# Kernel optimization log

Measured on AMD Instinct MI355X. Metric: run time of the kernel, lower is better.

The kernel has to match this reference:

```python
import jax, jax.numpy as jnp
import numpy as np

B, S, H = 32, 2048, 1024
STDV = 0.1


def setup_inputs() -> dict:
    key = jax.random.key(0)
    ks = jax.random.split(key, 8)
    u = lambda k, shape: jax.random.uniform(k, shape, minval=-STDV, maxval=STDV, dtype=jnp.float32)
    return {
        "inputs": jax.random.normal(ks[0], (B, S, H), dtype=jnp.float32),
        "qvector": jax.random.normal(ks[1], (B, H), dtype=jnp.float32),
        "W_u_1": u(ks[2], (H, H)),
        "W_u_m_1": u(ks[3], (H, H)),
        "W_u_h_1": u(ks[4], (H, 1)),
        "W_u_2": u(ks[5], (H, H)),
        "W_u_m_2": u(ks[6], (H, H)),
        "W_u_h_2": u(ks[7], (H, 1)),
    }


def reference(inputs, qvector, W_u_1, W_u_m_1, W_u_h_1, W_u_2, W_u_m_2, W_u_h_2):
    # inputs: [B, S, H], qvector: [B, H]
    def hop(m, W, Wm, Wh):
        # M = tanh(inputs @ W) gated by tanh(m @ Wm)  -> [B, S, H]
        M = jnp.tanh(jnp.einsum("bsh,hd->bsd", inputs, W))
        M = M * jnp.tanh(m @ Wm)[:, None, :]
        U = jnp.einsum("bsd,do->bso", M, Wh)        # [B, S, 1]
        alpha = jax.nn.softmax(U, axis=1)           # softmax over sequence
        return jnp.sum(inputs * alpha, axis=1)      # [B, H]

    mean_in = jnp.mean(inputs, axis=1)              # [B, H]
    u_att0 = mean_in
    m0 = mean_in * qvector
    u_att1 = hop(m0, W_u_1, W_u_m_1, W_u_h_1)
    m1 = m0 + u_att0 * qvector
    u_att2 = hop(m1, W_u_2, W_u_m_2, W_u_h_2)
    # original returns list [u_att0, u_att1, u_att2]; stack for a single array
    return jnp.stack([u_att0, u_att1, u_att2])      # [3, B, H]
```

## Files before the change

kernel.cpp:

```cpp
#include <hip/hip_runtime.h>
#include <hip/hip_bf16.h>
#include <math.h>

#define B_  32
#define S_  2048
#define H_  1024
#define M_TOT (B_ * S_)

typedef __bf16 bf16x8 __attribute__((ext_vector_type(8)));
typedef float  f32x4  __attribute__((ext_vector_type(4)));

__device__ __forceinline__ unsigned short f2bf(float f) {
    union { float f; unsigned int u; } v; v.f = f;
    unsigned int u = v.u;
    return (unsigned short)((u + 0x7fffu + ((u >> 16) & 1u)) >> 16);
}

__device__ __forceinline__ float bf2f(unsigned short s) {
    return __uint_as_float(((unsigned int)s) << 16);
}

__device__ __forceinline__ float fast_tanh(float x) {
    float e = __expf(2.0f * x);
    return 1.0f - 2.0f / (e + 1.0f);
}

__global__ void k_meanconv(const float* __restrict__ x,
                           unsigned short* __restrict__ xbf,
                           float* __restrict__ meanOut ) {
    int b  = blockIdx.x;
    int sc = blockIdx.y;
    int t  = threadIdx.x;
    size_t base = ((size_t)b * S_ + (size_t)sc * 32) * H_;
    const float4* xr = (const float4*)(x + base);
    ushort4* xo = (ushort4*)(xbf + base);
    float a0 = 0.f, a1 = 0.f, a2 = 0.f, a3 = 0.f;
    for (int s = 0; s < 32; ++s) {
        float4 v = xr[(size_t)s * 256 + t];
        a0 += v.x; a1 += v.y; a2 += v.z; a3 += v.w;
        ushort4 o;
        o.x = f2bf(v.x); o.y = f2bf(v.y); o.z = f2bf(v.z); o.w = f2bf(v.w);
        xo[(size_t)s * 256 + t] = o;
    }
    const float scl = 1.0f / (float)S_;
    float* mp = meanOut + b * H_ + t * 4;
    atomicAdd(mp + 0, a0 * scl);
    atomicAdd(mp + 1, a1 * scl);
    atomicAdd(mp + 2, a2 * scl);
    atomicAdd(mp + 3, a3 * scl);
}

__global__ void k_wconv(const float* __restrict__ W1,
                        const float* __restrict__ W2,
                        unsigned short* __restrict__ WT) {
    int n = blockIdx.x;
    int t = threadIdx.x;
    const float* src = (n < H_) ? (W1 + n) : (W2 + (n - H_));
    unsigned short* dst = WT + (size_t)n * H_;
    for (int kk = 0; kk < 4; ++kk) {
        int k = t + kk * 256;
        dst[k] = f2bf(src[(size_t)k * H_]);
    }
}

__global__ void k_vpart(const float* __restrict__ meanIn,
                        const float* __restrict__ q,
                        const float* __restrict__ Wm1,
                        const float* __restrict__ Wm2,
                        float* __restrict__ vtmp ) {
    int b   = blockIdx.x;
    int hop = blockIdx.y;
    int hc  = blockIdx.z;
    int t   = threadIdx.x;
    __shared__ float mL[128];
    float scale = (hop == 0) ? 1.0f : 2.0f;
    int h0 = hc * 128;
    if (t < 128)
        mL[t] = meanIn[b * H_ + h0 + t] * q[b * H_ + h0 + t] * scale;
    __syncthreads();
    const float* Wm = hop ? Wm2 : Wm1;
    int d0 = t * 4;
    float a0 = 0.f, a1 = 0.f, a2 = 0.f, a3 = 0.f;
    for (int h = 0; h < 128; ++h) {
        float m = mL[h];
        float4 w = *(const float4*)(Wm + (size_t)(h0 + h) * H_ + d0);
        a0 += m * w.x; a1 += m * w.y; a2 += m * w.z; a3 += m * w.w;
    }
    float* vo = vtmp + b * 2048 + hop * H_ + d0;
    atomicAdd(vo + 0, a0);
    atomicAdd(vo + 1, a1);
    atomicAdd(vo + 2, a2);
    atomicAdd(vo + 3, a3);
}

__global__ void k_vfin(const float* __restrict__ vtmp,
                       const float* __restrict__ Wh1,
                       const float* __restrict__ Wh2,
                       float* __restrict__ vcat) {
    int i = blockIdx.x * 256 + threadIdx.x;
    int hop = (i >> 10) & 1;
    int d = i & 1023;
    const float* Wh = hop ? Wh2 : Wh1;
    vcat[i] = tanhf(vtmp[i]) * Wh[d];
}

__global__ __launch_bounds__(256) void k_gemm(const unsigned short* __restrict__ Xbf,
                                              const unsigned short* __restrict__ WT,
                                              const float* __restrict__ vcat,
                                              float* __restrict__ U ) {
    int nt = blockIdx.x;
    int mt = blockIdx.y;
    int m0 = mt * 128;
    int n0 = nt * 128;
    int t    = threadIdx.x;
    int lane = t & 63;
    int wave = t >> 6;
    int wm = wave >> 1, wn = wave & 1;
    int fr = lane & 15;
    int fq = lane >> 4;

    __shared__ unsigned short As[128 * 32];
    __shared__ unsigned short Bs[128 * 32];

    f32x4 acc[4][4];
#pragma unroll
    for (int i = 0; i < 4; ++i)
#pragma unroll
        for (int j = 0; j < 4; ++j)
#pragma unroll
            for (int r = 0; r < 4; ++r) acc[i][j][r] = 0.0f;

    int idx0 = t, idx1 = t + 256;
    int row0 = idx0 >> 2, kc0 = ((idx0 & 3) - ((row0 >> 1) & 3)) & 3;
    int row1 = idx1 >> 2, kc1 = ((idx1 & 3) - ((row1 >> 1) & 3)) & 3;
    const unsigned short* gA0 = Xbf + (size_t)(m0 + row0) * H_ + kc0 * 8;
    const unsigned short* gA1 = Xbf + (size_t)(m0 + row1) * H_ + kc1 * 8;
    const unsigned short* gB0 = WT  + (size_t)(n0 + row0) * H_ + kc0 * 8;
    const unsigned short* gB1 = WT  + (size_t)(n0 + row1) * H_ + kc1 * 8;
    unsigned short* lA0 = As + idx0 * 8;
    unsigned short* lA1 = As + idx1 * 8;
    unsigned short* lB0 = Bs + idx0 * 8;
    unsigned short* lB1 = Bs + idx1 * 8;

    int slotR = (fq + ((fr >> 1) & 3)) & 3;
    const bf16x8* pa[4];
    const bf16x8* pb[4];
#pragma unroll
    for (int i = 0; i < 4; ++i)
        pa[i] = (const bf16x8*)(As + ((wm * 64 + i * 16 + fr) * 4 + slotR) * 8);
#pragma unroll
    for (int j = 0; j < 4; ++j)
        pb[j] = (const bf16x8*)(Bs + ((wn * 64 + j * 16 + fr) * 4 + slotR) * 8);

    for (int k0 = 0; k0 < H_; k0 += 32) {
        __builtin_amdgcn_global_load_lds((const __attribute__((address_space(1))) void*)(gA0 + k0),
                                         (__attribute__((address_space(3))) void*)lA0, 16, 0, 0);
        __builtin_amdgcn_global_load_lds((const __attribute__((address_space(1))) void*)(gA1 + k0),
                                         (__attribute__((address_space(3))) void*)lA1, 16, 0, 0);
        __builtin_amdgcn_global_load_lds((const __attribute__((address_space(1))) void*)(gB0 + k0),
                                         (__attribute__((address_space(3))) void*)lB0, 16, 0, 0);
        __builtin_amdgcn_global_load_lds((const __attribute__((address_space(1))) void*)(gB1 + k0),
                                         (__attribute__((address_space(3))) void*)lB1, 16, 0, 0);
        __syncthreads();
        bf16x8 af[4], bg[4];
#pragma unroll
        for (int i = 0; i < 4; ++i) af[i] = *pa[i];
#pragma unroll
        for (int j = 0; j < 4; ++j) bg[j] = *pb[j];
#pragma unroll
        for (int i = 0; i < 4; ++i)
#pragma unroll
            for (int j = 0; j < 4; ++j)
                acc[i][j] = __builtin_amdgcn_mfma_f32_16x16x32_bf16(af[i], bg[j], acc[i][j], 0, 0, 0);
        __syncthreads();
    }

    int b   = m0 >> 11;
    int hop = n0 >> 10;
    float vv[4];
#pragma unroll
    for (int j = 0; j < 4; ++j)
        vv[j] = vcat[b * 2048 + n0 + wn * 64 + j * 16 + fr];

#pragma unroll
    for (int i = 0; i < 4; ++i) {
#pragma unroll
        for (int r = 0; r < 4; ++r) {
            float sum = fast_tanh(acc[i][0][r]) * vv[0]
                      + fast_tanh(acc[i][1][r]) * vv[1]
                      + fast_tanh(acc[i][2][r]) * vv[2]
                      + fast_tanh(acc[i][3][r]) * vv[3];
            sum += __shfl_xor(sum, 1);
            sum += __shfl_xor(sum, 2);
            sum += __shfl_xor(sum, 4);
            sum += __shfl_xor(sum, 8);
            if (fr == 0) {
                int row = m0 + wm * 64 + i * 16 + fq * 4 + r;
                atomicAdd(&U[(size_t)hop * M_TOT + row], sum);
            }
        }
    }
}

__global__ void k_softmax(const float* __restrict__ U, float* __restrict__ alpha) {
    int id  = blockIdx.x;
    int hop = id >> 5, b = id & 31;
    int t = threadIdx.x;
    const float* u = U + (size_t)hop * M_TOT + (size_t)b * S_;
    float* al = alpha + (size_t)hop * M_TOT + (size_t)b * S_;
    float v[8];
    float mx = -1e30f;
#pragma unroll
    for (int i = 0; i < 8; ++i) { v[i] = u[t + i * 256]; mx = fmaxf(mx, v[i]); }
    __shared__ float red[256];
    red[t] = mx; __syncthreads();
    for (int s = 128; s > 0; s >>= 1) {
        if (t < s) red[t] = fmaxf(red[t], red[t + s]);
        __syncthreads();
    }
    mx = red[0]; __syncthreads();
    float sum = 0.f;
#pragma unroll
    for (int i = 0; i < 8; ++i) { v[i] = expf(v[i] - mx); sum += v[i]; }
    red[t] = sum; __syncthreads();
    for (int s = 128; s > 0; s >>= 1) {
        if (t < s) red[t] += red[t + s];
        __syncthreads();
    }
    float inv = 1.0f / red[0];
#pragma unroll
    for (int i = 0; i < 8; ++i) al[t + i * 256] = v[i] * inv;
}

__global__ void k_wsum(const unsigned short* __restrict__ Xbf,
                       const float* __restrict__ alpha,
                       float* __restrict__ out1 ,
                       float* __restrict__ out2 ) {
    int b  = blockIdx.x;
    int sc = blockIdx.y;
    int t  = threadIdx.x;
    __shared__ float a1[32], a2[32];
    int s0 = sc * 32;
    if (t < 32)       a1[t]      = alpha[(size_t)b * S_ + s0 + t];
    else if (t < 64)  a2[t - 32] = alpha[(size_t)M_TOT + (size_t)b * S_ + s0 + (t - 32)];
    __syncthreads();
    const ushort4* xr = (const ushort4*)(Xbf + ((size_t)b * S_ + s0) * H_);
    float x0a = 0.f, x1a = 0.f, x2a = 0.f, x3a = 0.f;
    float x0b = 0.f, x1b = 0.f, x2b = 0.f, x3b = 0.f;
    for (int s = 0; s < 32; ++s) {
        ushort4 u = xr[(size_t)s * 256 + t];
        float f0 = bf2f(u.x), f1 = bf2f(u.y), f2 = bf2f(u.z), f3 = bf2f(u.w);
        float w1 = a1[s], w2 = a2[s];
        x0a += f0 * w1; x1a += f1 * w1; x2a += f2 * w1; x3a += f3 * w1;
        x0b += f0 * w2; x1b += f1 * w2; x2b += f2 * w2; x3b += f3 * w2;
    }
    float* o1 = out1 + b * H_ + t * 4;
    float* o2 = out2 + b * H_ + t * 4;
    atomicAdd(o1 + 0, x0a); atomicAdd(o1 + 1, x1a);
    atomicAdd(o1 + 2, x2a); atomicAdd(o1 + 3, x3a);
    atomicAdd(o2 + 0, x0b); atomicAdd(o2 + 1, x1b);
    atomicAdd(o2 + 2, x2b); atomicAdd(o2 + 3, x3b);
}

extern "C" void kernel_launch(void* const* d_in, const int* in_sizes, int n_in,
                              void* d_out, int out_size, void* d_ws, size_t ws_size,
                              hipStream_t stream) {
    const float* inputs = (const float*)d_in[0];
    const float* q      = (const float*)d_in[1];
    const float* W1     = (const float*)d_in[2];
    const float* Wm1    = (const float*)d_in[3];
    const float* Wh1    = (const float*)d_in[4];
    const float* W2     = (const float*)d_in[5];
    const float* Wm2    = (const float*)d_in[6];
    const float* Wh2    = (const float*)d_in[7];
    float* out = (float*)d_out;

    char* ws = (char*)d_ws;
    unsigned short* Xbf  = (unsigned short*)(ws);
    unsigned short* WT   = (unsigned short*)(ws + 134217728);
    float*          vcat = (float*)(ws + 138412032);
    float*          U    = (float*)(ws + 138674176);
    float*          alph = (float*)(ws + 139198464);
    float*          vtmp = (float*)(ws + 139722752);

    hipMemsetAsync(d_out, 0, (size_t)out_size * sizeof(float), stream);
    hipMemsetAsync(U, 0, 524288 + 524288 + 262144, stream);

    k_meanconv<<<dim3(32, 64), 256, 0, stream>>>(inputs, Xbf, out);
    k_wconv  <<<dim3(2048),    256, 0, stream>>>(W1, W2, WT);
    k_vpart  <<<dim3(32, 2, 8), 256, 0, stream>>>(out, q, Wm1, Wm2, vtmp);
    k_vfin   <<<dim3(256),     256, 0, stream>>>(vtmp, Wh1, Wh2, vcat);
    k_gemm   <<<dim3(16, 512), 256, 0, stream>>>(Xbf, WT, vcat, U);
    k_softmax<<<dim3(64),      256, 0, stream>>>(U, alph);
    k_wsum   <<<dim3(32, 64),  256, 0, stream>>>(Xbf, alph, out + 32768, out + 65536);
}
```

Measured before the change: 871.7 us.

## Rewrite fused tanh GEMM as 256x256 double-buffered, phase-interleaved MFMA pipeline

The main bf16 GEMM now uses 256x256 tiles with 8 waves, a K-step of 64 and double-buffered LDS filled by direct global-to-LDS loads. Each K-step is split into four MFMA quadrants, with the next stage's loads interleaved between them and explicit waitcnt, barrier and setprio scheduling. Blocks are remapped so that neighbouring blocks share A and B tiles in cache. The aim is to hide memory latency behind MFMA work and raise arithmetic intensity, at the cost of more registers, 128 KB of LDS, and fragile hand-tuned synchronisation.

```diff
diff --git a/kernel.cpp b/kernel.cpp
--- a/kernel.cpp
+++ b/kernel.cpp
@@ -104,76 +104,51 @@
     vcat[i] = tanhf(vtmp[i]) * Wh[d];
 }
 
-__global__ __launch_bounds__(256) void k_gemm(const unsigned short* __restrict__ Xbf,
-                                              const unsigned short* __restrict__ WT,
-                                              const float* __restrict__ vcat,
-                                              float* __restrict__ U ) {
-    int nt = blockIdx.x;
-    int mt = blockIdx.y;
-    int m0 = mt * 128;
-    int n0 = nt * 128;
+__global__ __launch_bounds__(512, 2) void k_gemm(const unsigned short* __restrict__ Xbf,
+                                                 const unsigned short* __restrict__ WT,
+                                                 const float* __restrict__ vcat,
+                                                 float* __restrict__ U ) {
+    int raw = blockIdx.x;
+    int wg  = (raw & 7) * 256 + (raw >> 3);
+    int nt = wg & 7;
+    int mt = wg >> 3;
+    int m0 = mt * 256;
+    int n0 = nt * 256;
+
     int t    = threadIdx.x;
     int lane = t & 63;
     int wave = t >> 6;
-    int wm = wave >> 1, wn = wave & 1;
+    int wm = wave >> 2;
+    int wn = wave & 3;
     int fr = lane & 15;
     int fq = lane >> 4;
-
-    __shared__ unsigned short As[128 * 32];
-    __shared__ unsigned short Bs[128 * 32];
-
-    f32x4 acc[4][4];
-#pragma unroll
-    for (int i = 0; i < 4; ++i)
-#pragma unroll
-        for (int j = 0; j < 4; ++j)
-#pragma unroll
-            for (int r = 0; r < 4; ++r) acc[i][j][r] = 0.0f;
-
-    int idx0 = t, idx1 = t + 256;
-    int row0 = idx0 >> 2, kc0 = ((idx0 & 3) - ((row0 >> 1) & 3)) & 3;
-    int row1 = idx1 >> 2, kc1 = ((idx1 & 3) - ((row1 >> 1) & 3)) & 3;
-    const unsigned short* gA0 = Xbf + (size_t)(m0 + row0) * H_ + kc0 * 8;
-    const unsigned short* gA1 = Xbf + (size_t)(m0 + row1) * H_ + kc1 * 8;
-    const unsigned short* gB0 = WT  + (size_t)(n0 + row0) * H_ + kc0 * 8;
-    const unsigned short* gB1 = WT  + (size_t)(n0 + row1) * H_ + kc1 * 8;
-    unsigned short* lA0 = As + idx0 * 8;
-    unsigned short* lA1 = As + idx1 * 8;
-    unsigned short* lB0 = Bs + idx0 * 8;
-    unsigned short* lB1 = Bs + idx1 * 8;
-
-    int slotR = (fq + ((fr >> 1) & 3)) & 3;
-    const bf16x8* pa[4];
-    const bf16x8* pb[4];
-#pragma unroll
-    for (int i = 0; i < 4; ++i)
-        pa[i] = (const bf16x8*)(As + ((wm * 64 + i * 16 + fr) * 4 + slotR) * 8);
-#pragma unroll
-    for (int j = 0; j < 4; ++j)
-        pb[j] = (const bf16x8*)(Bs + ((wn * 64 + j * 16 + fr) * 4 + slotR) * 8);
-
-    for (int k0 = 0; k0 < H_; k0 += 32) {
-        __builtin_amdgcn_global_load_lds((const __attribute__((address_space(1))) void*)(gA0 + k0),
-                                         (__attribute__((address_space(3))) void*)lA0, 16, 0, 0);
-        __builtin_amdgcn_global_load_lds((const __attribute__((address_space(1))) void*)(gA1 + k0),
-                                         (__attribute__((address_space(3))) void*)lA1, 16, 0, 0);
-        __builtin_amdgcn_global_load_lds((const __attribute__((address_space(1))) void*)(gB0 + k0),
-                                         (__attribute__((address_space(3))) void*)lB0, 16, 0, 0);
-        __builtin_amdgcn_global_load_lds((const __attribute__((address_space(1))) void*)(gB1 + k0),
-                                         (__attribute__((address_space(3))) void*)lB1, 16, 0, 0);
-        __syncthreads();
-        bf16x8 af[4], bg[4];
-#pragma unroll
-        for (int i = 0; i < 4; ++i) af[i] = *pa[i];
-#pragma unroll
-        for (int j = 0; j < 4; ++j) bg[j] = *pb[j];
-#pragma unroll
-        for (int i = 0; i < 4; ++i)
-#pragma unroll
-            for (int j = 0; j < 4; ++j)
-                acc[i][j] = __builtin_amdgcn_mfma_f32_16x16x32_bf16(af[i], bg[j], acc[i][j], 0, 0, 0);
-        __syncthreads();
-    }
+    int s0 = (fq + fr) & 7;
+
+    __shared__ unsigned short lds[2][2][256 * 64];
+
+    const unsigned short* gA[4];
+    const unsigned short* gB[4];
+#pragma unroll
+    for (int L = 0; L < 4; ++L) {
+        int idx  = L * 512 + t;
+        int row  = idx >> 3;
+        int cst  = idx & 7;
+        int csrc = (cst - row) & 7;
+        gA[L] = Xbf + (size_t)(m0 + row) * H_ + csrc * 8;
+        gB[L] = WT  + (size_t)(n0 + row) * H_ + csrc * 8;
+    }
+
+#define STG_A(buf_, L_, v_) __builtin_amdgcn_global_load_lds( \
+        (const __attribute__((address_space(1))) void*)(gA[L_] + (v_) * 64), \
+        (__attribute__((address_space(3))) void*)(&lds[buf_][0][(L_) * 4096 + t * 8]), 16, 0, 0)
+#define STG_B(buf_, L_, v_) __builtin_amdgcn_global_load_lds( \
+        (const __attribute__((address_space(1))) void*)(gB[L_] + (v_) * 64), \
+        (__attribute__((address_space(3))) void*)(&lds[buf_][1][(L_) * 4096 + t * 8]), 16, 0, 0)
+
+#define ARD(buf_, QM_, i_, kk_) \
+    (*(const bf16x8*)&lds[buf_][0][(wm * 128 + (QM_) * 64 + (i_) * 16 + fr) * 64 + (s0 ^ ((kk_) * 4)) * 8])
+#define BRD(buf_, QN_, j_, kk_) \
+    (*(const bf16x8*)&lds[buf_][1][(wn * 64 + (QN_) * 32 + (j_) * 16 + fr) * 64 + (s0 ^ ((kk_) * 4)) * 8])
 
     int b   = m0 >> 11;
     int hop = n0 >> 10;
@@ -182,24 +157,125 @@
     for (int j = 0; j < 4; ++j)
         vv[j] = vcat[b * 2048 + n0 + wn * 64 + j * 16 + fr];
 
-#pragma unroll
-    for (int i = 0; i < 4; ++i) {
+    f32x4 acc[8][4];
+#pragma unroll
+    for (int i = 0; i < 8; ++i)
+#pragma unroll
+        for (int j = 0; j < 4; ++j)
+#pragma unroll
+            for (int r = 0; r < 4; ++r) acc[i][j][r] = 0.0f;
+
+    STG_A(0, 0, 0); STG_A(0, 1, 0); STG_A(0, 2, 0); STG_A(0, 3, 0);
+    STG_B(0, 0, 0); STG_B(0, 1, 0); STG_B(0, 2, 0); STG_B(0, 3, 0);
+    STG_A(1, 0, 1); STG_A(1, 1, 1); STG_A(1, 2, 1); STG_A(1, 3, 1);
+    STG_B(1, 0, 1); STG_B(1, 1, 1); STG_B(1, 2, 1); STG_B(1, 3, 1);
+    asm volatile("s_waitcnt vmcnt(8)" ::: "memory");
+    __builtin_amdgcn_s_barrier();
+    __builtin_amdgcn_sched_barrier(0);
+
+    bf16x8 a[4][2];
+    bf16x8 b0[2][2], b1[2][2];
+
+#pragma unroll 2
+    for (int v = 0; v < 16; ++v) {
+        int cur = v & 1;
+        bool sN2 = (v <= 13);
+
+#pragma unroll
+        for (int i = 0; i < 4; ++i) { a[i][0] = ARD(cur, 0, i, 0); a[i][1] = ARD(cur, 0, i, 1); }
+#pragma unroll
+        for (int j = 0; j < 2; ++j) { b0[j][0] = BRD(cur, 0, j, 0); b0[j][1] = BRD(cur, 0, j, 1); }
+        __builtin_amdgcn_sched_barrier(0);
+        __builtin_amdgcn_s_barrier();
+        asm volatile("s_waitcnt lgkmcnt(0)" ::: "memory");
+        __builtin_amdgcn_sched_barrier(0);
+        __builtin_amdgcn_s_setprio(1);
+#pragma unroll
+        for (int i = 0; i < 4; ++i)
+#pragma unroll
+            for (int j = 0; j < 2; ++j) {
+                acc[i][j] = __builtin_amdgcn_mfma_f32_16x16x32_bf16(a[i][0], b0[j][0], acc[i][j], 0, 0, 0);
+                acc[i][j] = __builtin_amdgcn_mfma_f32_16x16x32_bf16(a[i][1], b0[j][1], acc[i][j], 0, 0, 0);
+            }
+        __builtin_amdgcn_s_setprio(0);
+        __builtin_amdgcn_s_barrier();
+
+#pragma unroll
+        for (int j = 0; j < 2; ++j) { b1[j][0] = BRD(cur, 1, j, 0); b1[j][1] = BRD(cur, 1, j, 1); }
+        if (sN2) { STG_A(cur, 0, v + 2); STG_A(cur, 2, v + 2); }
+        __builtin_amdgcn_sched_barrier(0);
+        __builtin_amdgcn_s_barrier();
+        asm volatile("s_waitcnt lgkmcnt(0)" ::: "memory");
+        __builtin_amdgcn_sched_barrier(0);
+        __builtin_amdgcn_s_setprio(1);
+#pragma unroll
+        for (int i = 0; i < 4; ++i)
+#pragma unroll
+            for (int j = 0; j < 2; ++j) {
+                acc[i][2 + j] = __builtin_amdgcn_mfma_f32_16x16x32_bf16(a[i][0], b1[j][0], acc[i][2 + j], 0, 0, 0);
+                acc[i][2 + j] = __builtin_amdgcn_mfma_f32_16x16x32_bf16(a[i][1], b1[j][1], acc[i][2 + j], 0, 0, 0);
+            }
+        __builtin_amdgcn_s_setprio(0);
+        __builtin_amdgcn_s_barrier();
+
+#pragma unroll
+        for (int i = 0; i < 4; ++i) { a[i][0] = ARD(cur, 1, i, 0); a[i][1] = ARD(cur, 1, i, 1); }
+        if (sN2) { STG_B(cur, 0, v + 2); STG_B(cur, 1, v + 2); }
+        __builtin_amdgcn_sched_barrier(0);
+        __builtin_amdgcn_s_barrier();
+        asm volatile("s_waitcnt lgkmcnt(0)" ::: "memory");
+        __builtin_amdgcn_sched_barrier(0);
+        __builtin_amdgcn_s_setprio(1);
+#pragma unroll
+        for (int i = 0; i < 4; ++i)
+#pragma unroll
+            for (int j = 0; j < 2; ++j) {
+                acc[4 + i][j] = __builtin_amdgcn_mfma_f32_16x16x32_bf16(a[i][0], b0[j][0], acc[4 + i][j], 0, 0, 0);
+                acc[4 + i][j] = __builtin_amdgcn_mfma_f32_16x16x32_bf16(a[i][1], b0[j][1], acc[4 + i][j], 0, 0, 0);
+            }
+        __builtin_amdgcn_s_setprio(0);
+        __builtin_amdgcn_s_barrier();
+
+        if (sN2) { STG_B(cur, 2, v + 2); STG_B(cur, 3, v + 2); STG_A(cur, 1, v + 2); STG_A(cur, 3, v + 2); }
+        __builtin_amdgcn_sched_barrier(0);
+        __builtin_amdgcn_s_barrier();
+        __builtin_amdgcn_s_setprio(1);
+#pragma unroll
+        for (int i = 0; i < 4; ++i)
+#pragma unroll
+            for (int j = 0; j < 2; ++j) {
+                acc[4 + i][2 + j] = __builtin_amdgcn_mfma_f32_16x16x32_bf16(a[i][0], b1[j][0], acc[4 + i][2 + j], 0, 0, 0);
+                acc[4 + i][2 + j] = __builtin_amdgcn_mfma_f32_16x16x32_bf16(a[i][1], b1[j][1], acc[4 + i][2 + j], 0, 0, 0);
+            }
+        __builtin_amdgcn_s_setprio(0);
+        if (sN2) { asm volatile("s_waitcnt vmcnt(8)" ::: "memory"); }
+        else     { asm volatile("s_waitcnt vmcnt(0)" ::: "memory"); }
+        __builtin_amdgcn_s_barrier();
+        __builtin_amdgcn_sched_barrier(0);
+    }
+
+#pragma unroll
+    for (int i8 = 0; i8 < 8; ++i8) {
 #pragma unroll
         for (int r = 0; r < 4; ++r) {
-            float sum = fast_tanh(acc[i][0][r]) * vv[0]
-                      + fast_tanh(acc[i][1][r]) * vv[1]
-                      + fast_tanh(acc[i][2][r]) * vv[2]
-                      + fast_tanh(acc[i][3][r]) * vv[3];
+            float sum = fast_tanh(acc[i8][0][r]) * vv[0]
+                      + fast_tanh(acc[i8][1][r]) * vv[1]
+                      + fast_tanh(acc[i8][2][r]) * vv[2]
+                      + fast_tanh(acc[i8][3][r]) * vv[3];
             sum += __shfl_xor(sum, 1);
             sum += __shfl_xor(sum, 2);
             sum += __shfl_xor(sum, 4);
             sum += __shfl_xor(sum, 8);
             if (fr == 0) {
-                int row = m0 + wm * 64 + i * 16 + fq * 4 + r;
+                int row = m0 + wm * 128 + i8 * 16 + fq * 4 + r;
                 atomicAdd(&U[(size_t)hop * M_TOT + row], sum);
             }
         }
     }
+#undef STG_A
+#undef STG_B
+#undef ARD
+#undef BRD
 }
 
 __global__ void k_softmax(const float* __restrict__ U, float* __restrict__ alpha) {
@@ -290,7 +366,7 @@
     k_wconv  <<<dim3(2048),    256, 0, stream>>>(W1, W2, WT);
     k_vpart  <<<dim3(32, 2, 8), 256, 0, stream>>>(out, q, Wm1, Wm2, vtmp);
     k_vfin   <<<dim3(256),     256, 0, stream>>>(vtmp, Wh1, Wh2, vcat);
-    k_gemm   <<<dim3(16, 512), 256, 0, stream>>>(Xbf, WT, vcat, U);
+    k_gemm   <<<dim3(2048),    512, 0, stream>>>(Xbf, WT, vcat, U);
     k_softmax<<<dim3(64),      256, 0, stream>>>(U, alph);
     k_wsum   <<<dim3(32, 64),  256, 0, stream>>>(Xbf, alph, out + 32768, out + 65536);
 }
```

Result: faster. 843.5 us (-3.2%).
